# Performance work log

Hardware: AMD Instinct MI355X
Metric: run time of the kernel (lower is better)

## Reference

```python
import jax, jax.numpy as jnp
import numpy as np
import math

B, S, H = 1, 2048, 2048
NH, R = 16, 4            # num_heads, reduction_factor
KVH = NH // R            # reduced kv heads
HD = H // NH             # head_dim = 128
WIN = 128                # window_size
NEG = float('-inf')


def _masks(s):
    i = jnp.arange(s)[:, None]
    j = jnp.arange(s)[None, :]
    causal = jnp.where(j > i, NEG, 0.0).astype(jnp.float32)          # (S,S)
    local = jnp.where(jnp.abs(i - j) <= WIN // 2, 0.0, NEG).astype(jnp.float32)
    return causal, local


def setup_inputs() -> dict:
    key = jax.random.key(0)
    ks = jax.random.split(key, 7)
    sc = 1.0 / math.sqrt(H)
    return {
        'hidden_states': jax.random.normal(ks[0], (B, S, H), jnp.float32),
        'Wq': jax.random.normal(ks[1], (H, H), jnp.float32) * sc,
        'Wk': jax.random.normal(ks[2], (H, H // R), jnp.float32) * sc,
        'Wv': jax.random.normal(ks[3], (H, H // R), jnp.float32) * sc,
        'Wo': jax.random.normal(ks[4], (H, H), jnp.float32) * sc,
        'gate_w': jax.random.normal(ks[5], (H, 1), jnp.float32) * sc,
        'gate_b': jnp.zeros((1,), jnp.float32),
        'ln_g': jnp.ones((H,), jnp.float32),
        'ln_b': jnp.zeros((H,), jnp.float32),
    }


def _forward(hidden_states, Wq, Wk, Wv, Wo, gate_w, gate_b, ln_g, ln_b):
    b, s, _ = hidden_states.shape
    # gate: LayerNorm -> linear -> clamp -> sigmoid
    mu = jnp.mean(hidden_states, axis=-1, keepdims=True)
    var = jnp.var(hidden_states, axis=-1, keepdims=True)
    gi = (hidden_states - mu) * jax.lax.rsqrt(var + 1e-5) * ln_g + ln_b
    gates = jax.nn.sigmoid(jnp.clip(gi @ gate_w + gate_b, -10.0, 10.0))  # (b,s,1)

    q = (hidden_states @ Wq).reshape(b, s, NH, HD).transpose(0, 2, 1, 3)   # (b,NH,s,hd)
    k = (hidden_states @ Wk).reshape(b, s, KVH, HD).transpose(0, 2, 1, 3)  # (b,KVH,s,hd)
    v = (hidden_states @ Wv).reshape(b, s, KVH, HD).transpose(0, 2, 1, 3)
    # torch .repeat tiles the kv heads: head h uses kv head h % KVH
    k = jnp.tile(k, (1, R, 1, 1))
    v = jnp.tile(v, (1, R, 1, 1))

    scores = jnp.einsum('bhqd,bhkd->bhqk', q, k) / math.sqrt(HD)
    causal, local = _masks(s)
    local_p = jax.nn.softmax(scores + local, axis=-1)
    global_p = jax.nn.softmax(scores + causal, axis=-1)

    g = gates[:, None, :, :]  # (b,1,s,1): per-query gate, broadcast over heads/keys
    attn_probs = g * local_p + (1.0 - g) * global_p
    attn_out = jnp.einsum('bhqk,bhkd->bhqd', attn_probs, v)
    attn_out = attn_out.transpose(0, 2, 1, 3).reshape(b, s, H)
    output = attn_out @ Wo

    # regularization loss on gates (means over expanded tensor == per-token means)
    eps = 1e-5
    gf = gates
    gc = jnp.clip(gf, eps, 1.0 - eps)
    binary_reg = -0.1 * jnp.mean(gf * (1.0 - gf))
    entropy_reg = -0.01 * jnp.mean(gf * jnp.log(gc) + (1.0 - gf) * jnp.log(1.0 - gc))
    sparsity_reg = 0.1 * jnp.mean(gf)
    reg_loss = binary_reg + entropy_reg + sparsity_reg
    return output, reg_loss


def reference(hidden_states, Wq, Wk, Wv, Wo, gate_w, gate_b, ln_g, ln_b):
    return _forward(hidden_states, Wq, Wk, Wv, Wo, gate_w, gate_b, ln_g, ln_b)
```

## Files before the change

### kernel.cpp

```cpp
#include <hip/hip_runtime.h>
#include <hip/hip_bf16.h>
#include <math.h>

typedef __bf16 bf16_t;
typedef bf16_t bf16x8 __attribute__((ext_vector_type(8)));
typedef bf16_t bf16x4v __attribute__((ext_vector_type(4)));
typedef float f32x4 __attribute__((ext_vector_type(4)));

#define S_LEN 2048
#define HDIM 2048
#define QKV_LD 3072

__device__ __forceinline__ void gload_lds16(const bf16_t* g, bf16_t* l) {
  __builtin_amdgcn_global_load_lds(
      (const __attribute__((address_space(1))) unsigned int*)g,
      (__attribute__((address_space(3))) unsigned int*)l, 16, 0, 0);
}

__global__ __launch_bounds__(256) void ln_gate_cast_kernel(const float* __restrict__ hs,
                                                           const float* __restrict__ gw,
                                                           const float* __restrict__ gb,
                                                           const float* __restrict__ lng,
                                                           const float* __restrict__ lnb,
                                                           float* __restrict__ gates,
                                                           bf16_t* __restrict__ hsb) {
  __shared__ float red[256];
  int row = blockIdx.x, tid = threadIdx.x;
  const float* x = hs + (size_t)row * HDIM;
  bf16_t* y = hsb + (size_t)row * HDIM;
  float4 v0 = ((const float4*)x)[tid];
  float4 v1 = ((const float4*)x)[tid + 256];
  bf16x4v o;
  o[0] = (bf16_t)v0.x; o[1] = (bf16_t)v0.y; o[2] = (bf16_t)v0.z; o[3] = (bf16_t)v0.w;
  ((bf16x4v*)y)[tid] = o;
  o[0] = (bf16_t)v1.x; o[1] = (bf16_t)v1.y; o[2] = (bf16_t)v1.z; o[3] = (bf16_t)v1.w;
  ((bf16x4v*)y)[tid + 256] = o;
  float s = v0.x + v0.y + v0.z + v0.w + v1.x + v1.y + v1.z + v1.w;
  float ss = v0.x * v0.x + v0.y * v0.y + v0.z * v0.z + v0.w * v0.w +
             v1.x * v1.x + v1.y * v1.y + v1.z * v1.z + v1.w * v1.w;
  red[tid] = s; __syncthreads();
  for (int off = 128; off > 0; off >>= 1) { if (tid < off) red[tid] += red[tid + off]; __syncthreads(); }
  s = red[0]; __syncthreads();
  red[tid] = ss; __syncthreads();
  for (int off = 128; off > 0; off >>= 1) { if (tid < off) red[tid] += red[tid + off]; __syncthreads(); }
  ss = red[0]; __syncthreads();
  float mean = s * (1.f / HDIM);
  float var = ss * (1.f / HDIM) - mean * mean;
  float rstd = rsqrtf(var + 1e-5f);
  float dot = 0.f;
#pragma unroll
  for (int half = 0; half < 2; ++half) {
    int i = tid * 4 + half * 1024;
    float4 v = half ? v1 : v0;
    float4 g = *(const float4*)(lng + i);
    float4 b = *(const float4*)(lnb + i);
    float4 w = *(const float4*)(gw + i);
    dot += ((v.x - mean) * rstd * g.x + b.x) * w.x;
    dot += ((v.y - mean) * rstd * g.y + b.y) * w.y;
    dot += ((v.z - mean) * rstd * g.z + b.z) * w.z;
    dot += ((v.w - mean) * rstd * g.w + b.w) * w.w;
  }
  red[tid] = dot; __syncthreads();
  for (int off = 128; off > 0; off >>= 1) { if (tid < off) red[tid] += red[tid + off]; __syncthreads(); }
  if (tid == 0) {
    float gi = red[0] + gb[0];
    gi = fminf(10.f, fmaxf(-10.f, gi));
    gates[row] = 1.f / (1.f + __expf(-gi));
  }
}

__global__ __launch_bounds__(256) void wqkv_trans_kernel(const float* __restrict__ Wq,
                                                         const float* __restrict__ Wk,
                                                         const float* __restrict__ Wv,
                                                         bf16_t* __restrict__ wt) {
  __shared__ float tile[32][33];
  int bx = blockIdx.x, k0 = blockIdx.y * 32;
  const float* src; int N, n0, o0;
  if (bx < 64)      { src = Wq; N = 2048; n0 = bx * 32;        o0 = n0; }
  else if (bx < 80) { src = Wk; N = 512;  n0 = (bx - 64) * 32; o0 = 2048 + n0; }
  else              { src = Wv; N = 512;  n0 = (bx - 80) * 32; o0 = 2560 + n0; }
  int tx = threadIdx.x & 31, ty = threadIdx.x >> 5;
#pragma unroll
  for (int i = 0; i < 4; ++i)
    tile[ty + i * 8][tx] = src[(size_t)(k0 + ty + i * 8) * N + n0 + tx];
  __syncthreads();
#pragma unroll
  for (int i = 0; i < 4; ++i)
    wt[(size_t)(o0 + ty + i * 8) * 2048 + k0 + tx] = (bf16_t)tile[tx][ty + i * 8];
}

__global__ __launch_bounds__(256) void transpose_cast_kernel(const float* __restrict__ in,
                                                             bf16_t* __restrict__ out,
                                                             int K, int N) {
  __shared__ float tile[32][33];
  int n0 = blockIdx.x * 32, k0 = blockIdx.y * 32;
  int tx = threadIdx.x & 31, ty = threadIdx.x >> 5;
#pragma unroll
  for (int i = 0; i < 4; ++i)
    tile[ty + i * 8][tx] = in[(size_t)(k0 + ty + i * 8) * N + n0 + tx];
  __syncthreads();
#pragma unroll
  for (int i = 0; i < 4; ++i)
    out[(size_t)(n0 + ty + i * 8) * K + k0 + tx] = (bf16_t)tile[tx][ty + i * 8];
}

__global__ __launch_bounds__(256) void vtrans_kernel(const bf16_t* __restrict__ qkv,
                                                     bf16_t* __restrict__ vt) {
  __shared__ bf16_t tile[32][33];
  int v0 = blockIdx.x * 32, s0 = blockIdx.y * 32;
  int tx = threadIdx.x & 31, ty = threadIdx.x >> 5;
#pragma unroll
  for (int i = 0; i < 4; ++i)
    tile[ty + i * 8][tx] = qkv[(size_t)(s0 + ty + i * 8) * QKV_LD + 2560 + v0 + tx];
  __syncthreads();
#pragma unroll
  for (int i = 0; i < 4; ++i)
    vt[(size_t)(v0 + ty + i * 8) * S_LEN + s0 + tx] = tile[tx][ty + i * 8];
}

__global__ __launch_bounds__(256) void reg_loss_kernel(const float* __restrict__ gates,
                                                       float* __restrict__ out) {
  __shared__ float red[256];
  int tid = threadIdx.x;
  float sb = 0.f, se = 0.f, sg = 0.f;
  for (int i = tid; i < S_LEN; i += 256) {
    float g = gates[i];
    float gc = fminf(1.f - 1e-5f, fmaxf(1e-5f, g));
    sb += g * (1.f - g);
    se += g * logf(gc) + (1.f - g) * logf(1.f - gc);
    sg += g;
  }
  red[tid] = sb; __syncthreads();
  for (int off = 128; off > 0; off >>= 1) { if (tid < off) red[tid] += red[tid + off]; __syncthreads(); }
  sb = red[0]; __syncthreads();
  red[tid] = se; __syncthreads();
  for (int off = 128; off > 0; off >>= 1) { if (tid < off) red[tid] += red[tid + off]; __syncthreads(); }
  se = red[0]; __syncthreads();
  red[tid] = sg; __syncthreads();
  for (int off = 128; off > 0; off >>= 1) { if (tid < off) red[tid] += red[tid + off]; __syncthreads(); }
  if (tid == 0) {
    const float inv = 1.f / (float)S_LEN;
    float reg = -0.1f * (sb * inv) - 0.01f * (se * inv) + 0.1f * (red[0] * inv);
    out[0] = reg;
  }
}

template <typename OutT>
__global__ __launch_bounds__(256) void gemm_bt_kernel(const bf16_t* __restrict__ A,
                                                      const bf16_t* __restrict__ Bt,
                                                      OutT* __restrict__ C,
                                                      int M, int N, int K) {
  __shared__ bf16_t As[2][128][32];
  __shared__ bf16_t Bs[2][128][32];
  int tid = threadIdx.x;
  int lane = tid & 63, wave = tid >> 6;
  int wr = wave >> 1, wc = wave & 1;
  int m0 = blockIdx.y * 128, n0 = blockIdx.x * 128;
  int lrow = lane & 15, lhi = lane >> 4;

  int srow = wave * 32 + (lane >> 2);
  int scol = (lane & 3) * 8;
  const bf16_t* Ag = A + (size_t)(m0 + srow) * K + scol;
  const bf16_t* Bg = Bt + (size_t)(n0 + srow) * K + scol;
  size_t row16 = (size_t)16 * K;

  f32x4 acc[4][4];
#pragma unroll
  for (int a = 0; a < 4; ++a)
#pragma unroll
    for (int b = 0; b < 4; ++b)
#pragma unroll
      for (int r = 0; r < 4; ++r) acc[a][b][r] = 0.f;

  gload_lds16(Ag, &As[0][wave * 32][0]);
  gload_lds16(Ag + row16, &As[0][wave * 32 + 16][0]);
  gload_lds16(Bg, &Bs[0][wave * 32][0]);
  gload_lds16(Bg + row16, &Bs[0][wave * 32 + 16][0]);
  __syncthreads();

  int cur = 0;
  for (int k0 = 0; k0 < K; k0 += 32) {
    int nxt = cur ^ 1;
    if (k0 + 32 < K) {
      gload_lds16(Ag + k0 + 32, &As[nxt][wave * 32][0]);
      gload_lds16(Ag + k0 + 32 + row16, &As[nxt][wave * 32 + 16][0]);
      gload_lds16(Bg + k0 + 32, &Bs[nxt][wave * 32][0]);
      gload_lds16(Bg + k0 + 32 + row16, &Bs[nxt][wave * 32 + 16][0]);
    }
    bf16x8 af[4], bfr[4];
#pragma unroll
    for (int a = 0; a < 4; ++a)
      af[a] = *(const bf16x8*)(&As[cur][wr * 64 + a * 16 + lrow][lhi * 8]);
#pragma unroll
    for (int b = 0; b < 4; ++b)
      bfr[b] = *(const bf16x8*)(&Bs[cur][wc * 64 + b * 16 + lrow][lhi * 8]);
    __builtin_amdgcn_s_setprio(1);
#pragma unroll
    for (int a = 0; a < 4; ++a)
#pragma unroll
      for (int b = 0; b < 4; ++b)
        acc[a][b] = __builtin_amdgcn_mfma_f32_16x16x32_bf16(af[a], bfr[b], acc[a][b], 0, 0, 0);
    __builtin_amdgcn_s_setprio(0);
    __syncthreads();
    cur = nxt;
  }
#pragma unroll
  for (int a = 0; a < 4; ++a)
#pragma unroll
    for (int b = 0; b < 4; ++b)
#pragma unroll
      for (int r = 0; r < 4; ++r) {
        int row = m0 + wr * 64 + a * 16 + lhi * 4 + r;
        int col = n0 + wc * 64 + b * 16 + lrow;
        C[(size_t)row * N + col] = (OutT)acc[a][b][r];
      }
}

__global__ __launch_bounds__(256, 2) void attn_kernel(const bf16_t* __restrict__ QKV,
                                                      const bf16_t* __restrict__ VTg,
                                                      const float* __restrict__ gates,
                                                      bf16_t* __restrict__ out) {
  __shared__ bf16_t Ks[2][64][128];
  __shared__ bf16_t Vt[2][128][64];
  __shared__ bf16_t Pw[4][16][72];

  int b = blockIdx.x;
  int h = b & 15;
  int t5 = b >> 4;
  int c = (t5 < 16) ? (31 - t5) : (t5 - 16);
  int q0c = c * 64;
  int tid = threadIdx.x;
  int lane = tid & 63, w = tid >> 6;
  int lrow = lane & 15, lhi = lane >> 4;
  int q0w = q0c + w * 16;
  int hk = h & 3;
  const bf16_t* Qp = QKV + h * 128;
  const bf16_t* Kp = QKV + 2048 + hk * 128;
  const bf16_t* Vt_g = VTg + (size_t)hk * 128 * S_LEN;

  bf16x8 aq[4];
#pragma unroll
  for (int ks = 0; ks < 4; ++ks)
    aq[ks] = *(const bf16x8*)(Qp + (size_t)(q0w + lrow) * QKV_LD + ks * 32 + lhi * 8);

  float lg[4], ll[4];
  f32x4 og[8], ol[8];
#pragma unroll
  for (int r = 0; r < 4; ++r) { lg[r] = ll[r] = 0.f; }
#pragma unroll
  for (int d = 0; d < 8; ++d)
#pragma unroll
    for (int r = 0; r < 4; ++r) { og[d][r] = 0.f; ol[d][r] = 0.f; }

  const float NEGINF = -__builtin_inff();
  const float scl = 0.08838834764831845f;
  const float MFIX = 8.0f;
  int kend = q0c + 128;
  if (kend > S_LEN) kend = S_LEN;
  int nt = kend >> 6;

  int kr = tid >> 4, c16 = tid & 15;
  int vr = tid >> 3, c8 = tid & 7;

  {
    bf16x8 kreg[4], vreg[4];
#pragma unroll
    for (int i = 0; i < 4; ++i)
      kreg[i] = *(const bf16x8*)(Kp + (size_t)(kr + i * 16) * QKV_LD + c16 * 8);
#pragma unroll
    for (int i = 0; i < 4; ++i)
      vreg[i] = *(const bf16x8*)(Vt_g + (size_t)(vr + i * 32) * S_LEN + c8 * 8);
#pragma unroll
    for (int i = 0; i < 4; ++i) {
      int rr = kr + i * 16;
      *(bf16x8*)(&Ks[0][rr][(c16 ^ (rr & 7)) * 8]) = kreg[i];
    }
#pragma unroll
    for (int i = 0; i < 4; ++i) {
      int rr = vr + i * 32;
      *(bf16x8*)(&Vt[0][rr][(c8 ^ (rr & 7)) * 8]) = vreg[i];
    }
  }
  __syncthreads();

  for (int ti = 0; ti < nt; ++ti) {
    int k0 = ti << 6;
    int bufc = ti & 1, bufn = bufc ^ 1;
    bool more = (ti + 1 < nt);

    bf16x8 kreg[4], vreg[4];
    if (more) {
      int k0n = k0 + 64;
#pragma unroll
      for (int i = 0; i < 4; ++i)
        kreg[i] = *(const bf16x8*)(Kp + (size_t)(k0n + kr + i * 16) * QKV_LD + c16 * 8);
#pragma unroll
      for (int i = 0; i < 4; ++i)
        vreg[i] = *(const bf16x8*)(Vt_g + (size_t)(vr + i * 32) * S_LEN + k0n + c8 * 8);
    }

    f32x4 sc[4];
#pragma unroll
    for (int t = 0; t < 4; ++t) {
#pragma unroll
      for (int r = 0; r < 4; ++r) sc[t][r] = 0.f;
    }
#pragma unroll
    for (int t = 0; t < 4; ++t) {
      int n = t * 16 + lrow;
      int swz = n & 7;
#pragma unroll
      for (int ks = 0; ks < 4; ++ks) {
        bf16x8 bk = *(const bf16x8*)(&Ks[bufc][n][((ks * 4 + lhi) ^ swz) * 8]);
        sc[t] = __builtin_amdgcn_mfma_f32_16x16x32_bf16(aq[ks], bk, sc[t], 0, 0, 0);
      }
    }

    bool g_act = (k0 <= q0w + 15);
    bool g_full = (k0 + 63 <= q0w);
    bool l_act = (k0 + 63 >= q0w - 64) && (k0 <= q0w + 79);

    if (g_act) {
#pragma unroll
      for (int r = 0; r < 4; ++r) {
        int i = q0w + lhi * 4 + r;
        float v0, v1, v2, v3;
        if (g_full) {
          v0 = sc[0][r] * scl; v1 = sc[1][r] * scl;
          v2 = sc[2][r] * scl; v3 = sc[3][r] * scl;
        } else {
          int j = k0 + lrow;
          v0 = (j > i) ? NEGINF : sc[0][r] * scl;
          v1 = (j + 16 > i) ? NEGINF : sc[1][r] * scl;
          v2 = (j + 32 > i) ? NEGINF : sc[2][r] * scl;
          v3 = (j + 48 > i) ? NEGINF : sc[3][r] * scl;
        }
        float p0 = __expf(v0 - MFIX), p1 = __expf(v1 - MFIX);
        float p2 = __expf(v2 - MFIX), p3 = __expf(v3 - MFIX);
        int pr = lhi * 4 + r;
        Pw[w][pr][lrow] = (bf16_t)p0;
        Pw[w][pr][16 + lrow] = (bf16_t)p1;
        Pw[w][pr][32 + lrow] = (bf16_t)p2;
        Pw[w][pr][48 + lrow] = (bf16_t)p3;
        lg[r] += (p0 + p1) + (p2 + p3);
      }
      bf16x8 ap0 = *(const bf16x8*)(&Pw[w][lrow][lhi * 8]);
      bf16x8 ap1 = *(const bf16x8*)(&Pw[w][lrow][32 + lhi * 8]);
#pragma unroll
      for (int d = 0; d < 8; ++d) {
        int drow = d * 16 + lrow;
        int swz = drow & 7;
        bf16x8 bv0 = *(const bf16x8*)(&Vt[bufc][drow][(lhi ^ swz) * 8]);
        bf16x8 bv1 = *(const bf16x8*)(&Vt[bufc][drow][((4 + lhi) ^ swz) * 8]);
        og[d] = __builtin_amdgcn_mfma_f32_16x16x32_bf16(ap0, bv0, og[d], 0, 0, 0);
        og[d] = __builtin_amdgcn_mfma_f32_16x16x32_bf16(ap1, bv1, og[d], 0, 0, 0);
      }
    }

    if (l_act) {
#pragma unroll
      for (int r = 0; r < 4; ++r) {
        int i = q0w + lhi * 4 + r;
        int j = k0 + lrow;
        int d0 = i - j, d1 = d0 - 16, d2 = d0 - 32, d3 = d0 - 48;
        float v0 = (d0 > 64 || d0 < -64) ? NEGINF : sc[0][r] * scl;
        float v1 = (d1 > 64 || d1 < -64) ? NEGINF : sc[1][r] * scl;
        float v2 = (d2 > 64 || d2 < -64) ? NEGINF : sc[2][r] * scl;
        float v3 = (d3 > 64 || d3 < -64) ? NEGINF : sc[3][r] * scl;
        float p0 = __expf(v0 - MFIX), p1 = __expf(v1 - MFIX);
        float p2 = __expf(v2 - MFIX), p3 = __expf(v3 - MFIX);
        int pr = lhi * 4 + r;
        Pw[w][pr][lrow] = (bf16_t)p0;
        Pw[w][pr][16 + lrow] = (bf16_t)p1;
        Pw[w][pr][32 + lrow] = (bf16_t)p2;
        Pw[w][pr][48 + lrow] = (bf16_t)p3;
        ll[r] += (p0 + p1) + (p2 + p3);
      }
      bf16x8 ap0 = *(const bf16x8*)(&Pw[w][lrow][lhi * 8]);
      bf16x8 ap1 = *(const bf16x8*)(&Pw[w][lrow][32 + lhi * 8]);
#pragma unroll
      for (int d = 0; d < 8; ++d) {
        int drow = d * 16 + lrow;
        int swz = drow & 7;
        bf16x8 bv0 = *(const bf16x8*)(&Vt[bufc][drow][(lhi ^ swz) * 8]);
        bf16x8 bv1 = *(const bf16x8*)(&Vt[bufc][drow][((4 + lhi) ^ swz) * 8]);
        ol[d] = __builtin_amdgcn_mfma_f32_16x16x32_bf16(ap0, bv0, ol[d], 0, 0, 0);
        ol[d] = __builtin_amdgcn_mfma_f32_16x16x32_bf16(ap1, bv1, ol[d], 0, 0, 0);
      }
    }

    if (more) {
#pragma unroll
      for (int i = 0; i < 4; ++i) {
        int rr = kr + i * 16;
        *(bf16x8*)(&Ks[bufn][rr][(c16 ^ (rr & 7)) * 8]) = kreg[i];
      }
#pragma unroll
      for (int i = 0; i < 4; ++i) {
        int rr = vr + i * 32;
        *(bf16x8*)(&Vt[bufn][rr][(c8 ^ (rr & 7)) * 8]) = vreg[i];
      }
    }
    __syncthreads();
  }

#pragma unroll
  for (int r = 0; r < 4; ++r) {
#pragma unroll
    for (int m = 1; m < 16; m <<= 1) {
      lg[r] += __shfl_xor(lg[r], m, 64);
      ll[r] += __shfl_xor(ll[r], m, 64);
    }
  }

#pragma unroll
  for (int r = 0; r < 4; ++r) {
    int i = q0w + lhi * 4 + r;
    float gv = gates[i];
    float il = 1.f / ll[r], ig = 1.f / lg[r];
#pragma unroll
    for (int d = 0; d < 8; ++d)
      out[(size_t)i * HDIM + h * 128 + d * 16 + lrow] =
          (bf16_t)(gv * ol[d][r] * il + (1.f - gv) * og[d][r] * ig);
  }
}

extern "C" void kernel_launch(void* const* d_in, const int* in_sizes, int n_in,
                              void* d_out, int out_size, void* d_ws, size_t ws_size,
                              hipStream_t stream) {
  const float* hs  = (const float*)d_in[0];
  const float* Wq  = (const float*)d_in[1];
  const float* Wk  = (const float*)d_in[2];
  const float* Wv  = (const float*)d_in[3];
  const float* Wo  = (const float*)d_in[4];
  const float* gw  = (const float*)d_in[5];
  const float* gb  = (const float*)d_in[6];
  const float* lng = (const float*)d_in[7];
  const float* lnb = (const float*)d_in[8];
  float* out = (float*)d_out;

  char* ws = (char*)d_ws;
  bf16_t* hsb   = (bf16_t*)(ws);
  bf16_t* wt    = (bf16_t*)(ws + 8388608);
  bf16_t* wot   = (bf16_t*)(ws + 20971520);
  bf16_t* qkv   = (bf16_t*)(ws + 29360128);
  bf16_t* ao    = (bf16_t*)(ws + 41943040);
  float*  gates = (float*)(ws + 50331648);
  bf16_t* vtb   = (bf16_t*)(ws + 50339840);

  ln_gate_cast_kernel<<<2048, 256, 0, stream>>>(hs, gw, gb, lng, lnb, gates, hsb);
  wqkv_trans_kernel<<<dim3(96, 64), 256, 0, stream>>>(Wq, Wk, Wv, wt);
  transpose_cast_kernel<<<dim3(64, 64), 256, 0, stream>>>(Wo, wot, 2048, 2048);
  reg_loss_kernel<<<1, 256, 0, stream>>>(gates, out + (size_t)4194304);

  gemm_bt_kernel<bf16_t><<<dim3(24, 16), 256, 0, stream>>>(hsb, wt, qkv, 2048, 3072, 2048);

  vtrans_kernel<<<dim3(16, 64), 256, 0, stream>>>(qkv, vtb);

  attn_kernel<<<dim3(512), 256, 0, stream>>>(qkv, vtb, gates, ao);

  gemm_bt_kernel<float><<<dim3(16, 16), 256, 0, stream>>>(ao, wot, out, 2048, 2048, 2048);
}
```

Baseline: 182.2 us.

## Triple-buffer GEMM loads, merge weight transposes, share V fragments in attention

The GEMM moves from a double-buffered LDS pipeline to a three-stage ring with explicit vmcnt waits and raw barriers, so global-to-LDS loads run two tiles ahead of compute. The Wq/Wk/Wv and Wo transpose-cast kernels are merged into one launch. In attention, the V tile fragments are read from LDS once and shared by the global and local probability MFMAs instead of being loaded twice. The costs are more LDS per GEMM block, which may reduce occupancy, and extra live registers for the held probability fragments.

```diff
diff --git a/kernel.cpp b/kernel.cpp
--- a/kernel.cpp
+++ b/kernel.cpp
@@ -69,16 +69,19 @@
   }
 }
 
-__global__ __launch_bounds__(256) void wqkv_trans_kernel(const float* __restrict__ Wq,
+__global__ __launch_bounds__(256) void wall_trans_kernel(const float* __restrict__ Wq,
                                                          const float* __restrict__ Wk,
                                                          const float* __restrict__ Wv,
-                                                         bf16_t* __restrict__ wt) {
+                                                         const float* __restrict__ Wo,
+                                                         bf16_t* __restrict__ wt,
+                                                         bf16_t* __restrict__ wot) {
   __shared__ float tile[32][33];
   int bx = blockIdx.x, k0 = blockIdx.y * 32;
-  const float* src; int N, n0, o0;
-  if (bx < 64)      { src = Wq; N = 2048; n0 = bx * 32;        o0 = n0; }
-  else if (bx < 80) { src = Wk; N = 512;  n0 = (bx - 64) * 32; o0 = 2048 + n0; }
-  else              { src = Wv; N = 512;  n0 = (bx - 80) * 32; o0 = 2560 + n0; }
+  const float* src; int N, n0; bf16_t* dst; int o0;
+  if (bx < 64)      { src = Wq; N = 2048; n0 = bx * 32;        dst = wt;  o0 = n0; }
+  else if (bx < 80) { src = Wk; N = 512;  n0 = (bx - 64) * 32; dst = wt;  o0 = 2048 + n0; }
+  else if (bx < 96) { src = Wv; N = 512;  n0 = (bx - 80) * 32; dst = wt;  o0 = 2560 + n0; }
+  else              { src = Wo; N = 2048; n0 = (bx - 96) * 32; dst = wot; o0 = n0; }
   int tx = threadIdx.x & 31, ty = threadIdx.x >> 5;
 #pragma unroll
   for (int i = 0; i < 4; ++i)
@@ -86,22 +89,7 @@
   __syncthreads();
 #pragma unroll
   for (int i = 0; i < 4; ++i)
-    wt[(size_t)(o0 + ty + i * 8) * 2048 + k0 + tx] = (bf16_t)tile[tx][ty + i * 8];
-}
-
-__global__ __launch_bounds__(256) void transpose_cast_kernel(const float* __restrict__ in,
-                                                             bf16_t* __restrict__ out,
-                                                             int K, int N) {
-  __shared__ float tile[32][33];
-  int n0 = blockIdx.x * 32, k0 = blockIdx.y * 32;
-  int tx = threadIdx.x & 31, ty = threadIdx.x >> 5;
-#pragma unroll
-  for (int i = 0; i < 4; ++i)
-    tile[ty + i * 8][tx] = in[(size_t)(k0 + ty + i * 8) * N + n0 + tx];
-  __syncthreads();
-#pragma unroll
-  for (int i = 0; i < 4; ++i)
-    out[(size_t)(n0 + ty + i * 8) * K + k0 + tx] = (bf16_t)tile[tx][ty + i * 8];
+    dst[(size_t)(o0 + ty + i * 8) * 2048 + k0 + tx] = (bf16_t)tile[tx][ty + i * 8];
 }
 
 __global__ __launch_bounds__(256) void vtrans_kernel(const bf16_t* __restrict__ qkv,
@@ -150,8 +138,8 @@
                                                       const bf16_t* __restrict__ Bt,
                                                       OutT* __restrict__ C,
                                                       int M, int N, int K) {
-  __shared__ bf16_t As[2][128][32];
-  __shared__ bf16_t Bs[2][128][32];
+  __shared__ bf16_t As[3][128][32];
+  __shared__ bf16_t Bs[3][128][32];
   int tid = threadIdx.x;
   int lane = tid & 63, wave = tid >> 6;
   int wr = wave >> 1, wc = wave & 1;
@@ -172,21 +160,25 @@
 #pragma unroll
       for (int r = 0; r < 4; ++r) acc[a][b][r] = 0.f;
 
-  gload_lds16(Ag, &As[0][wave * 32][0]);
-  gload_lds16(Ag + row16, &As[0][wave * 32 + 16][0]);
-  gload_lds16(Bg, &Bs[0][wave * 32][0]);
-  gload_lds16(Bg + row16, &Bs[0][wave * 32 + 16][0]);
-  __syncthreads();
-
-  int cur = 0;
-  for (int k0 = 0; k0 < K; k0 += 32) {
-    int nxt = cur ^ 1;
-    if (k0 + 32 < K) {
-      gload_lds16(Ag + k0 + 32, &As[nxt][wave * 32][0]);
-      gload_lds16(Ag + k0 + 32 + row16, &As[nxt][wave * 32 + 16][0]);
-      gload_lds16(Bg + k0 + 32, &Bs[nxt][wave * 32][0]);
-      gload_lds16(Bg + k0 + 32 + row16, &Bs[nxt][wave * 32 + 16][0]);
-    }
+  auto stage = [&](int t, int bufi) {
+    int k0 = t * 32;
+    gload_lds16(Ag + k0, &As[bufi][wave * 32][0]);
+    gload_lds16(Ag + k0 + row16, &As[bufi][wave * 32 + 16][0]);
+    gload_lds16(Bg + k0, &Bs[bufi][wave * 32][0]);
+    gload_lds16(Bg + k0 + row16, &Bs[bufi][wave * 32 + 16][0]);
+  };
+
+  int T = K >> 5;
+  stage(0, 0);
+  stage(1, 1);
+  asm volatile("s_waitcnt vmcnt(4)" ::: "memory");
+  __builtin_amdgcn_s_barrier();
+  __builtin_amdgcn_sched_barrier(0);
+
+  for (int t = 0; t < T; ++t) {
+    int cur = t % 3;
+    bool issue = (t + 2 < T);
+    if (issue) stage(t + 2, (t + 2) % 3);
     bf16x8 af[4], bfr[4];
 #pragma unroll
     for (int a = 0; a < 4; ++a)
@@ -201,8 +193,14 @@
       for (int b = 0; b < 4; ++b)
         acc[a][b] = __builtin_amdgcn_mfma_f32_16x16x32_bf16(af[a], bfr[b], acc[a][b], 0, 0, 0);
     __builtin_amdgcn_s_setprio(0);
-    __syncthreads();
-    cur = nxt;
+    __builtin_amdgcn_sched_barrier(0);
+    if (issue) {
+      asm volatile("s_waitcnt vmcnt(4)" ::: "memory");
+    } else {
+      asm volatile("s_waitcnt vmcnt(0)" ::: "memory");
+    }
+    __builtin_amdgcn_s_barrier();
+    __builtin_amdgcn_sched_barrier(0);
   }
 #pragma unroll
   for (int a = 0; a < 4; ++a)
@@ -319,6 +317,8 @@
     bool g_act = (k0 <= q0w + 15);
     bool g_full = (k0 + 63 <= q0w);
     bool l_act = (k0 + 63 >= q0w - 64) && (k0 <= q0w + 79);
+
+    bf16x8 apg0, apg1, apl0, apl1;
 
     if (g_act) {
 #pragma unroll
@@ -344,17 +344,8 @@
         Pw[w][pr][48 + lrow] = (bf16_t)p3;
         lg[r] += (p0 + p1) + (p2 + p3);
       }
-      bf16x8 ap0 = *(const bf16x8*)(&Pw[w][lrow][lhi * 8]);
-      bf16x8 ap1 = *(const bf16x8*)(&Pw[w][lrow][32 + lhi * 8]);
-#pragma unroll
-      for (int d = 0; d < 8; ++d) {
-        int drow = d * 16 + lrow;
-        int swz = drow & 7;
-        bf16x8 bv0 = *(const bf16x8*)(&Vt[bufc][drow][(lhi ^ swz) * 8]);
-        bf16x8 bv1 = *(const bf16x8*)(&Vt[bufc][drow][((4 + lhi) ^ swz) * 8]);
-        og[d] = __builtin_amdgcn_mfma_f32_16x16x32_bf16(ap0, bv0, og[d], 0, 0, 0);
-        og[d] = __builtin_amdgcn_mfma_f32_16x16x32_bf16(ap1, bv1, og[d], 0, 0, 0);
-      }
+      apg0 = *(const bf16x8*)(&Pw[w][lrow][lhi * 8]);
+      apg1 = *(const bf16x8*)(&Pw[w][lrow][32 + lhi * 8]);
     }
 
     if (l_act) {
@@ -376,16 +367,25 @@
         Pw[w][pr][48 + lrow] = (bf16_t)p3;
         ll[r] += (p0 + p1) + (p2 + p3);
       }
-      bf16x8 ap0 = *(const bf16x8*)(&Pw[w][lrow][lhi * 8]);
-      bf16x8 ap1 = *(const bf16x8*)(&Pw[w][lrow][32 + lhi * 8]);
+      apl0 = *(const bf16x8*)(&Pw[w][lrow][lhi * 8]);
+      apl1 = *(const bf16x8*)(&Pw[w][lrow][32 + lhi * 8]);
+    }
+
+    if (g_act || l_act) {
 #pragma unroll
       for (int d = 0; d < 8; ++d) {
         int drow = d * 16 + lrow;
         int swz = drow & 7;
         bf16x8 bv0 = *(const bf16x8*)(&Vt[bufc][drow][(lhi ^ swz) * 8]);
         bf16x8 bv1 = *(const bf16x8*)(&Vt[bufc][drow][((4 + lhi) ^ swz) * 8]);
-        ol[d] = __builtin_amdgcn_mfma_f32_16x16x32_bf16(ap0, bv0, ol[d], 0, 0, 0);
-        ol[d] = __builtin_amdgcn_mfma_f32_16x16x32_bf16(ap1, bv1, ol[d], 0, 0, 0);
+        if (g_act) {
+          og[d] = __builtin_amdgcn_mfma_f32_16x16x32_bf16(apg0, bv0, og[d], 0, 0, 0);
+          og[d] = __builtin_amdgcn_mfma_f32_16x16x32_bf16(apg1, bv1, og[d], 0, 0, 0);
+        }
+        if (l_act) {
+          ol[d] = __builtin_amdgcn_mfma_f32_16x16x32_bf16(apl0, bv0, ol[d], 0, 0, 0);
+          ol[d] = __builtin_amdgcn_mfma_f32_16x16x32_bf16(apl1, bv1, ol[d], 0, 0, 0);
+        }
       }
     }
 
@@ -449,8 +449,7 @@
   bf16_t* vtb   = (bf16_t*)(ws + 50339840);
 
   ln_gate_cast_kernel<<<2048, 256, 0, stream>>>(hs, gw, gb, lng, lnb, gates, hsb);
-  wqkv_trans_kernel<<<dim3(96, 64), 256, 0, stream>>>(Wq, Wk, Wv, wt);
-  transpose_cast_kernel<<<dim3(64, 64), 256, 0, stream>>>(Wo, wot, 2048, 2048);
+  wall_trans_kernel<<<dim3(160, 64), 256, 0, stream>>>(Wq, Wk, Wv, Wo, wt, wot);
   reg_loss_kernel<<<1, 256, 0, stream>>>(gates, out + (size_t)4194304);
 
   gemm_bt_kernel<bf16_t><<<dim3(24, 16), 256, 0, stream>>>(hsb, wt, qkv, 2048, 3072, 2048);
```

After: 190.2 us. +4.4%, slower.
